# Performance work log

Hardware: AMD Instinct MI355X
Metric: run time of the kernel (lower is better)

Reference implementation:

```python
import jax, jax.numpy as jnp
import numpy as np

N_HEADS = 16
R = 64  # number of latents; note: scale = r**-0.5 per original code


def setup_inputs() -> dict:
    key = jax.random.key(0)
    ks = jax.random.split(key, 8)
    B, S, D = 32, 4096, 1024
    s = D ** -0.5
    return {
        "x": jax.random.normal(ks[0], (B, S, D), dtype=jnp.float32),
        "wq": jax.random.normal(ks[1], (D, D), dtype=jnp.float32) * s,
        "kv_latent": jax.random.normal(ks[2], (R, D), dtype=jnp.float32),
        "wo": jax.random.normal(ks[3], (D, D), dtype=jnp.float32) * s,
        "w1": jax.random.normal(ks[4], (D, D), dtype=jnp.float32) * s,
        "b1": jnp.zeros((D,), dtype=jnp.float32),
        "w2": jax.random.normal(ks[5], (D, D), dtype=jnp.float32) * s,
        "b2": jnp.zeros((D,), dtype=jnp.float32),
    }


def reference(x, wq, kv_latent, wo, w1, b1, w2, b2):
    B, S, D = x.shape
    hd = D // N_HEADS
    scale = R ** -0.5
    q = x.reshape(-1, D)                                   # [N, D], N = B*S
    xq = (q @ wq).reshape(-1, N_HEADS, hd) * scale         # [N, H, hd]
    kv = kv_latent.reshape(R, N_HEADS, hd)                 # [R, H, hd]
    attn = jax.nn.softmax(jnp.einsum('nhd,rhd->nhr', xq, kv), axis=-1)
    out = jnp.einsum('nhr,rhd->nhd', attn, kv).reshape(-1, D)
    out = out @ wo                                         # [N, D]
    # residual MLP block (exact GELU, matching torch nn.GELU default)
    h = jax.nn.gelu(out @ w1 + b1, approximate=False)
    out = h @ w2 + b2 + out
    # mean-pool per segment; equal segments of length S -> equivalent to
    # block_diag(ones(l)/l) @ out without materializing the [B, N] mask
    return out.reshape(B, S, D).mean(axis=1)               # [B, D]
```

## Files before the change

kernel.cpp:

```cpp
#include <hip/hip_runtime.h>

using bf16x8 = __attribute__((ext_vector_type(8))) __bf16;
using f32x4  = __attribute__((ext_vector_type(4))) float;

#define AS1(p) ((const __attribute__((address_space(1))) void*)(p))
#define AS3(p) ((__attribute__((address_space(3))) void*)(p))

__device__ __forceinline__ unsigned short f2bf(float f) {
  unsigned u = __float_as_uint(f);
  u += 0x7fffu + ((u >> 16) & 1u);
  return (unsigned short)(u >> 16);
}
__device__ __forceinline__ float bf2f(unsigned short h) {
  return __uint_as_float(((unsigned)h) << 16);
}

__global__ __launch_bounds__(256) void transpose_w(
    const float* __restrict__ wq, const float* __restrict__ wo,
    const float* __restrict__ w1, const float* __restrict__ w2,
    unsigned short* __restrict__ wqT, unsigned short* __restrict__ woT,
    unsigned short* __restrict__ w1T, unsigned short* __restrict__ w2T) {
  __shared__ float tile[64][65];
  const int z = blockIdx.z;
  const float* src = z == 0 ? wq : z == 1 ? wo : z == 2 ? w1 : w2;
  unsigned short* dst = z == 0 ? wqT : z == 1 ? woT : z == 2 ? w1T : w2T;
  const int tx = threadIdx.x & 63, ty = threadIdx.x >> 6;
  const int n0 = blockIdx.x * 64, k0 = blockIdx.y * 64;
#pragma unroll
  for (int i = 0; i < 16; i++) {
    int k = ty * 16 + i;
    tile[k][tx] = src[(size_t)(k0 + k) * 1024 + n0 + tx];
  }
  __syncthreads();
#pragma unroll
  for (int i = 0; i < 16; i++) {
    int n = ty * 16 + i;
    dst[(size_t)(n0 + n) * 1024 + k0 + tx] = f2bf(tile[tx][n]);
  }
}

__global__ __launch_bounds__(256) void convert_kv(
    const float* __restrict__ kv, unsigned short* __restrict__ kvb,
    unsigned short* __restrict__ kvT) {
  int idx = blockIdx.x * 256 + threadIdx.x;
  kvb[idx] = f2bf(kv[idx]);
  int h = idx >> 12, d = (idx >> 6) & 63, r = idx & 63;
  kvT[idx] = f2bf(kv[r * 1024 + h * 64 + d]);
}

template <int EPI, bool AF32>
__global__ __launch_bounds__(256) void gemm128(
    const void* __restrict__ Ap, const unsigned short* __restrict__ BT,
    unsigned short* __restrict__ C, const float* __restrict__ bias,
    const unsigned short* __restrict__ resid, float* __restrict__ pool,
    float scale) {
  __shared__ unsigned short As[128 * 32];
  __shared__ unsigned short Bs[128 * 32];
  const int tid = threadIdx.x;
  const int lane = tid & 63, wave = tid >> 6;
  const int wr = wave >> 1, wc = wave & 1;
  const int l15 = lane & 15, l4 = lane >> 4;
  const int bid = blockIdx.y * 8 + blockIdx.x;
  const int xcd = bid & 7, j = bid >> 3;
  const int row0 = ((xcd << 7) | (j >> 3)) * 128;
  const int col0 = (j & 7) * 128;
  const int swz = (l15 >> 1) & 3;

  f32x4 acc[4][4];
#pragma unroll
  for (int i = 0; i < 4; i++)
#pragma unroll
    for (int jj = 0; jj < 4; jj++) acc[i][jj] = f32x4{0.f, 0.f, 0.f, 0.f};

  for (int k0 = 0; k0 < 1024; k0 += 32) {
    if (AF32) {
      const float* A = (const float*)Ap;
#pragma unroll
      for (int s = 0; s < 4; s++) {
        int c = tid + 256 * s;
        int r = c >> 3, c4 = c & 7;
        const float4 v = *(const float4*)(A + (size_t)(row0 + r) * 1024 + k0 + c4 * 4);
        ushort4 b;
        b.x = f2bf(v.x); b.y = f2bf(v.y); b.z = f2bf(v.z); b.w = f2bf(v.w);
        int cc = (c4 >> 1) ^ ((r >> 1) & 3), h = c4 & 1;
        *(ushort4*)(As + r * 32 + cc * 8 + h * 4) = b;
      }
    } else {
      const unsigned short* A = (const unsigned short*)Ap;
#pragma unroll
      for (int t = 0; t < 2; t++) {
        int p = wave * 128 + t * 64 + lane;
        int r = p >> 2, c = (p & 3) ^ ((r >> 1) & 3);
        __builtin_amdgcn_global_load_lds(AS1(A + (size_t)(row0 + r) * 1024 + k0 + c * 8),
                                         AS3(As + p * 8), 16, 0, 0);
      }
    }
#pragma unroll
    for (int t = 0; t < 2; t++) {
      int p = wave * 128 + t * 64 + lane;
      int r = p >> 2, c = (p & 3) ^ ((r >> 1) & 3);
      __builtin_amdgcn_global_load_lds(AS1(BT + (size_t)(col0 + r) * 1024 + k0 + c * 8),
                                       AS3(Bs + p * 8), 16, 0, 0);
    }
    __syncthreads();

    bf16x8 af[4], bfr[4];
#pragma unroll
    for (int i = 0; i < 4; i++)
      af[i] = *(const bf16x8*)(As + (wr * 64 + i * 16 + l15) * 32 + (l4 ^ swz) * 8);
#pragma unroll
    for (int jj = 0; jj < 4; jj++)
      bfr[jj] = *(const bf16x8*)(Bs + (wc * 64 + jj * 16 + l15) * 32 + (l4 ^ swz) * 8);
#pragma unroll
    for (int i = 0; i < 4; i++)
#pragma unroll
      for (int jj = 0; jj < 4; jj++)
        acc[i][jj] = __builtin_amdgcn_mfma_f32_16x16x32_bf16(af[i], bfr[jj], acc[i][jj], 0, 0, 0);
    __syncthreads();
  }

  if (EPI == 0) {
#pragma unroll
    for (int i = 0; i < 4; i++)
#pragma unroll
      for (int jj = 0; jj < 4; jj++)
#pragma unroll
        for (int v = 0; v < 4; v++) {
          int row = row0 + wr * 64 + i * 16 + l4 * 4 + v;
          int col = col0 + wc * 64 + jj * 16 + l15;
          C[(size_t)row * 1024 + col] = f2bf(acc[i][jj][v] * scale);
        }
  } else if (EPI == 1) {
#pragma unroll
    for (int jj = 0; jj < 4; jj++) {
      int col = col0 + wc * 64 + jj * 16 + l15;
      float bj = bias[col];
#pragma unroll
      for (int i = 0; i < 4; i++)
#pragma unroll
        for (int v = 0; v < 4; v++) {
          int row = row0 + wr * 64 + i * 16 + l4 * 4 + v;
          float val = acc[i][jj][v] + bj;
          float g = 0.5f * val * (1.0f + erff(val * 0.70710678118654752f));
          C[(size_t)row * 1024 + col] = f2bf(g);
        }
    }
  } else {
    float cs[4] = {0.f, 0.f, 0.f, 0.f};
#pragma unroll
    for (int jj = 0; jj < 4; jj++) {
      int col = col0 + wc * 64 + jj * 16 + l15;
      float bj = bias[col];
#pragma unroll
      for (int i = 0; i < 4; i++)
#pragma unroll
        for (int v = 0; v < 4; v++) {
          int row = row0 + wr * 64 + i * 16 + l4 * 4 + v;
          float val = acc[i][jj][v] + bj + bf2f(resid[(size_t)row * 1024 + col]);
          cs[jj] += val;
        }
    }
#pragma unroll
    for (int jj = 0; jj < 4; jj++) {
      cs[jj] += __shfl_xor(cs[jj], 16);
      cs[jj] += __shfl_xor(cs[jj], 32);
    }
    if (l4 == 0) {
      int b = row0 >> 12;
#pragma unroll
      for (int jj = 0; jj < 4; jj++) {
        int col = col0 + wc * 64 + jj * 16 + l15;
        atomicAdd(pool + b * 1024 + col, cs[jj] * (1.0f / 4096.0f));
      }
    }
  }
}

__global__ __launch_bounds__(256) void attn_kernel(
    const unsigned short* __restrict__ q, const unsigned short* __restrict__ kvb,
    const unsigned short* __restrict__ kvT, unsigned short* __restrict__ outp) {
  __shared__ unsigned short smem[32768];
  unsigned short* qs   = smem;
  unsigned short* kvs  = smem + 16384;
  unsigned short* kvTs = smem + 24576;
  const int tid = threadIdx.x;
  const int lane = tid & 63, wave = tid >> 6;
  const int wr = wave >> 1, wc = wave & 1;
  const int l15 = lane & 15, l4 = lane >> 4;
  const int hp = blockIdx.x, row0 = blockIdx.y * 128;

#pragma unroll
  for (int t = 0; t < 8; t++) {
    int c = wave * 512 + t * 64 + lane;
    int r = c >> 4, c8 = c & 15;
    __builtin_amdgcn_global_load_lds(AS1(q + (size_t)(row0 + r) * 1024 + hp * 128 + c8 * 8),
                                     AS3(qs + (wave * 512 + t * 64) * 8), 16, 0, 0);
  }
#pragma unroll
  for (int t = 0; t < 4; t++) {
    int c = wave * 256 + t * 64 + lane;
    int h = c >> 9, r = (c >> 3) & 63, c8 = c & 7;
    __builtin_amdgcn_global_load_lds(AS1(kvb + r * 1024 + (hp * 2 + h) * 64 + c8 * 8),
                                     AS3(kvs + (wave * 256 + t * 64) * 8), 16, 0, 0);
    __builtin_amdgcn_global_load_lds(AS1(kvT + (hp * 2 + h) * 4096 + (c & 511) * 8),
                                     AS3(kvTs + (wave * 256 + t * 64) * 8), 16, 0, 0);
  }
  __syncthreads();

  f32x4 sc[4][4];
#pragma unroll
  for (int i = 0; i < 4; i++)
#pragma unroll
    for (int j = 0; j < 4; j++) sc[i][j] = f32x4{0.f, 0.f, 0.f, 0.f};
#pragma unroll
  for (int ks = 0; ks < 2; ks++) {
    bf16x8 af[4], bfr[4];
#pragma unroll
    for (int i = 0; i < 4; i++)
      af[i] = *(const bf16x8*)(qs + (wr * 64 + i * 16 + l15) * 128 + wc * 64 + ks * 32 + l4 * 8);
#pragma unroll
    for (int j = 0; j < 4; j++)
      bfr[j] = *(const bf16x8*)(kvs + wc * 4096 + (j * 16 + l15) * 64 + ks * 32 + l4 * 8);
#pragma unroll
    for (int i = 0; i < 4; i++)
#pragma unroll
      for (int j = 0; j < 4; j++)
        sc[i][j] = __builtin_amdgcn_mfma_f32_16x16x32_bf16(af[i], bfr[j], sc[i][j], 0, 0, 0);
  }
  __syncthreads();

  unsigned short* attn = qs;
#pragma unroll
  for (int i = 0; i < 4; i++)
#pragma unroll
    for (int v = 0; v < 4; v++) {
      float m = fmaxf(fmaxf(sc[i][0][v], sc[i][1][v]), fmaxf(sc[i][2][v], sc[i][3][v]));
#pragma unroll
      for (int msk = 1; msk <= 8; msk <<= 1) m = fmaxf(m, __shfl_xor(m, msk));
      float e0 = __expf(sc[i][0][v] - m), e1 = __expf(sc[i][1][v] - m);
      float e2 = __expf(sc[i][2][v] - m), e3 = __expf(sc[i][3][v] - m);
      float s = e0 + e1 + e2 + e3;
#pragma unroll
      for (int msk = 1; msk <= 8; msk <<= 1) s += __shfl_xor(s, msk);
      float inv = 1.0f / s;
      int row = wr * 64 + i * 16 + l4 * 4 + v;
      attn[wc * 8192 + row * 64 + 0 * 16 + l15] = f2bf(e0 * inv);
      attn[wc * 8192 + row * 64 + 1 * 16 + l15] = f2bf(e1 * inv);
      attn[wc * 8192 + row * 64 + 2 * 16 + l15] = f2bf(e2 * inv);
      attn[wc * 8192 + row * 64 + 3 * 16 + l15] = f2bf(e3 * inv);
    }

  f32x4 o[4][4];
#pragma unroll
  for (int i = 0; i < 4; i++)
#pragma unroll
    for (int j = 0; j < 4; j++) o[i][j] = f32x4{0.f, 0.f, 0.f, 0.f};
#pragma unroll
  for (int ks = 0; ks < 2; ks++) {
    bf16x8 af[4], bfr[4];
#pragma unroll
    for (int i = 0; i < 4; i++)
      af[i] = *(const bf16x8*)(attn + wc * 8192 + (wr * 64 + i * 16 + l15) * 64 + ks * 32 + l4 * 8);
#pragma unroll
    for (int j = 0; j < 4; j++)
      bfr[j] = *(const bf16x8*)(kvTs + wc * 4096 + (j * 16 + l15) * 64 + ks * 32 + l4 * 8);
#pragma unroll
    for (int i = 0; i < 4; i++)
#pragma unroll
      for (int j = 0; j < 4; j++)
        o[i][j] = __builtin_amdgcn_mfma_f32_16x16x32_bf16(af[i], bfr[j], o[i][j], 0, 0, 0);
  }
#pragma unroll
  for (int i = 0; i < 4; i++)
#pragma unroll
    for (int j = 0; j < 4; j++)
#pragma unroll
      for (int v = 0; v < 4; v++) {
        int row = row0 + wr * 64 + i * 16 + l4 * 4 + v;
        int col = (hp * 2 + wc) * 64 + j * 16 + l15;
        outp[(size_t)row * 1024 + col] = f2bf(o[i][j][v]);
      }
}

extern "C" void kernel_launch(void* const* d_in, const int* in_sizes, int n_in,
                              void* d_out, int out_size, void* d_ws, size_t ws_size,
                              hipStream_t stream) {
  const float* x  = (const float*)d_in[0];
  const float* wq = (const float*)d_in[1];
  const float* kv = (const float*)d_in[2];
  const float* wo = (const float*)d_in[3];
  const float* w1 = (const float*)d_in[4];
  const float* b1 = (const float*)d_in[5];
  const float* w2 = (const float*)d_in[6];
  const float* b2 = (const float*)d_in[7];
  char* ws = (char*)d_ws;
  const size_t MB = 1024 * 1024;
  unsigned short* wqT = (unsigned short*)(ws + 0 * MB);
  unsigned short* woT = (unsigned short*)(ws + 2 * MB);
  unsigned short* w1T = (unsigned short*)(ws + 4 * MB);
  unsigned short* w2T = (unsigned short*)(ws + 6 * MB);
  unsigned short* kvb = (unsigned short*)(ws + 8 * MB);
  unsigned short* kvT = (unsigned short*)(ws + 8 * MB + 256 * 1024);
  unsigned short* buf1 = (unsigned short*)(ws + 16 * MB);
  unsigned short* buf2 = (unsigned short*)(ws + 16 * MB + 256 * MB);
  float* out = (float*)d_out;

  hipMemsetAsync(d_out, 0, (size_t)out_size * sizeof(float), stream);
  transpose_w<<<dim3(16, 16, 4), 256, 0, stream>>>(wq, wo, w1, w2, wqT, woT, w1T, w2T);
  convert_kv<<<256, 256, 0, stream>>>(kv, kvb, kvT);

  dim3 g(8, 1024);
  gemm128<0, true ><<<g, 256, 0, stream>>>(x, wqT, buf1, nullptr, nullptr, nullptr, 0.125f);
  attn_kernel<<<g, 256, 0, stream>>>(buf1, kvb, kvT, buf2);
  gemm128<0, false><<<g, 256, 0, stream>>>(buf2, woT, buf1, nullptr, nullptr, nullptr, 1.0f);
  gemm128<1, false><<<g, 256, 0, stream>>>(buf1, w1T, buf2, b1, nullptr, nullptr, 1.0f);
  gemm128<2, false><<<g, 256, 0, stream>>>(buf2, w2T, nullptr, b2, buf1, out, 1.0f);
}
```

Measured before the change: 2.438 ms.

## Replace 128x128 GEMM with double-buffered 256x256 tile GEMM and pre-convert x

Replaces the 128x128, 256-thread GEMM with a 256x256-tile, 512-thread kernel that uses a 64-wide K step, an XOR-swizzled LDS layout and double-buffered global-to-LDS loads overlapped with MFMA compute. Wave priority is raised around the MFMA bursts. The fp32 input x is now converted to bf16 by a separate kernel so every GEMM uses the async LDS load path. This targets low arithmetic intensity and exposed load latency, at the cost of an extra pass over x, 128 KB of LDS per block and higher register pressure.

Measured after the change: 2.348 ms. 3.7% less time.

```diff
diff --git a/kernel.cpp b/kernel.cpp
--- a/kernel.cpp
+++ b/kernel.cpp
@@ -48,99 +48,142 @@
   kvT[idx] = f2bf(kv[r * 1024 + h * 64 + d]);
 }
 
-template <int EPI, bool AF32>
-__global__ __launch_bounds__(256) void gemm128(
-    const void* __restrict__ Ap, const unsigned short* __restrict__ BT,
+__global__ __launch_bounds__(256) void convert_x(
+    const float4* __restrict__ x, ushort4* __restrict__ xb) {
+  size_t i = (size_t)blockIdx.x * 256 + threadIdx.x;
+  float4 v = x[i];
+  ushort4 b;
+  b.x = f2bf(v.x); b.y = f2bf(v.y); b.z = f2bf(v.z); b.w = f2bf(v.w);
+  xb[i] = b;
+}
+
+template <int EPI>
+__global__ __launch_bounds__(512, 2) void gemm256(
+    const unsigned short* __restrict__ A, const unsigned short* __restrict__ BT,
     unsigned short* __restrict__ C, const float* __restrict__ bias,
     const unsigned short* __restrict__ resid, float* __restrict__ pool,
     float scale) {
-  __shared__ unsigned short As[128 * 32];
-  __shared__ unsigned short Bs[128 * 32];
+  __shared__ unsigned short Asm[2 * 16384];
+  __shared__ unsigned short Bsm[2 * 16384];
   const int tid = threadIdx.x;
   const int lane = tid & 63, wave = tid >> 6;
-  const int wr = wave >> 1, wc = wave & 1;
+  const int wr = wave >> 2, wc = wave & 3;
   const int l15 = lane & 15, l4 = lane >> 4;
-  const int bid = blockIdx.y * 8 + blockIdx.x;
-  const int xcd = bid & 7, j = bid >> 3;
-  const int row0 = ((xcd << 7) | (j >> 3)) * 128;
-  const int col0 = (j & 7) * 128;
-  const int swz = (l15 >> 1) & 3;
-
-  f32x4 acc[4][4];
-#pragma unroll
-  for (int i = 0; i < 4; i++)
-#pragma unroll
-    for (int jj = 0; jj < 4; jj++) acc[i][jj] = f32x4{0.f, 0.f, 0.f, 0.f};
-
-  for (int k0 = 0; k0 < 1024; k0 += 32) {
-    if (AF32) {
-      const float* A = (const float*)Ap;
-#pragma unroll
-      for (int s = 0; s < 4; s++) {
-        int c = tid + 256 * s;
-        int r = c >> 3, c4 = c & 7;
-        const float4 v = *(const float4*)(A + (size_t)(row0 + r) * 1024 + k0 + c4 * 4);
-        ushort4 b;
-        b.x = f2bf(v.x); b.y = f2bf(v.y); b.z = f2bf(v.z); b.w = f2bf(v.w);
-        int cc = (c4 >> 1) ^ ((r >> 1) & 3), h = c4 & 1;
-        *(ushort4*)(As + r * 32 + cc * 8 + h * 4) = b;
-      }
-    } else {
-      const unsigned short* A = (const unsigned short*)Ap;
-#pragma unroll
-      for (int t = 0; t < 2; t++) {
-        int p = wave * 128 + t * 64 + lane;
-        int r = p >> 2, c = (p & 3) ^ ((r >> 1) & 3);
-        __builtin_amdgcn_global_load_lds(AS1(A + (size_t)(row0 + r) * 1024 + k0 + c * 8),
-                                         AS3(As + p * 8), 16, 0, 0);
-      }
-    }
-#pragma unroll
-    for (int t = 0; t < 2; t++) {
-      int p = wave * 128 + t * 64 + lane;
-      int r = p >> 2, c = (p & 3) ^ ((r >> 1) & 3);
-      __builtin_amdgcn_global_load_lds(AS1(BT + (size_t)(col0 + r) * 1024 + k0 + c * 8),
-                                       AS3(Bs + p * 8), 16, 0, 0);
-    }
-    __syncthreads();
-
-    bf16x8 af[4], bfr[4];
-#pragma unroll
-    for (int i = 0; i < 4; i++)
-      af[i] = *(const bf16x8*)(As + (wr * 64 + i * 16 + l15) * 32 + (l4 ^ swz) * 8);
-#pragma unroll
-    for (int jj = 0; jj < 4; jj++)
-      bfr[jj] = *(const bf16x8*)(Bs + (wc * 64 + jj * 16 + l15) * 32 + (l4 ^ swz) * 8);
-#pragma unroll
-    for (int i = 0; i < 4; i++)
-#pragma unroll
-      for (int jj = 0; jj < 4; jj++)
-        acc[i][jj] = __builtin_amdgcn_mfma_f32_16x16x32_bf16(af[i], bfr[jj], acc[i][jj], 0, 0, 0);
-    __syncthreads();
-  }
+
+  const int bid = blockIdx.x;
+  const int idx = bid >> 3;
+  const int row0 = ((bid & 7) * 64 + (idx >> 2)) * 256;
+  const int col0 = (idx & 3) * 256;
+
+  const unsigned short* aSrc[4];
+  const unsigned short* bSrc[4];
+#pragma unroll
+  for (int s = 0; s < 4; s++) {
+    int p = tid + 512 * s;
+    int r = p >> 3, c = (p & 7) ^ (r & 7);
+    aSrc[s] = A  + (size_t)(row0 + r) * 1024 + c * 8;
+    bSrc[s] = BT + (size_t)(col0 + r) * 1024 + c * 8;
+  }
+
+  auto stage = [&](int t, int b) {
+#pragma unroll
+    for (int s = 0; s < 4; s++)
+      __builtin_amdgcn_global_load_lds(AS1(aSrc[s] + t * 64),
+                                       AS3(Asm + b * 16384 + (tid + 512 * s) * 8), 16, 0, 0);
+#pragma unroll
+    for (int s = 0; s < 4; s++)
+      __builtin_amdgcn_global_load_lds(AS1(bSrc[s] + t * 64),
+                                       AS3(Bsm + b * 16384 + (tid + 512 * s) * 8), 16, 0, 0);
+  };
+
+  f32x4 acc[8][4];
+#pragma unroll
+  for (int i = 0; i < 8; i++)
+#pragma unroll
+    for (int j = 0; j < 4; j++) acc[i][j] = f32x4{0.f, 0.f, 0.f, 0.f};
+
+  int aOff[8], bOff[4];
+#pragma unroll
+  for (int i = 0; i < 8; i++) {
+    int ra = wr * 128 + i * 16 + l15;
+    aOff[i] = ra * 64 + ((l4 ^ (ra & 7)) * 8);
+  }
+#pragma unroll
+  for (int j = 0; j < 4; j++) {
+    int rb = wc * 64 + j * 16 + l15;
+    bOff[j] = rb * 64 + ((l4 ^ (rb & 7)) * 8);
+  }
+
+  auto compute = [&](int b) {
+#pragma unroll
+    for (int ks = 0; ks < 2; ks++) {
+      bf16x8 af[8], bfr[4];
+#pragma unroll
+      for (int i = 0; i < 8; i++)
+        af[i] = *(const bf16x8*)(Asm + b * 16384 + (aOff[i] ^ (ks * 32)));
+#pragma unroll
+      for (int j = 0; j < 4; j++)
+        bfr[j] = *(const bf16x8*)(Bsm + b * 16384 + (bOff[j] ^ (ks * 32)));
+      __builtin_amdgcn_s_setprio(1);
+#pragma unroll
+      for (int i = 0; i < 8; i++)
+#pragma unroll
+        for (int j = 0; j < 4; j++)
+          acc[i][j] = __builtin_amdgcn_mfma_f32_16x16x32_bf16(af[i], bfr[j], acc[i][j], 0, 0, 0);
+      __builtin_amdgcn_s_setprio(0);
+    }
+  };
+
+  stage(0, 0);
+  stage(1, 1);
+  asm volatile("s_waitcnt vmcnt(8)" ::: "memory");
+  __builtin_amdgcn_sched_barrier(0);
+  __builtin_amdgcn_s_barrier();
+  __builtin_amdgcn_sched_barrier(0);
+
+  int cur = 0;
+#pragma unroll 2
+  for (int t = 0; t < 14; ++t) {
+    compute(cur);
+    __builtin_amdgcn_sched_barrier(0);
+    __builtin_amdgcn_s_barrier();
+    __builtin_amdgcn_sched_barrier(0);
+    stage(t + 2, cur);
+    asm volatile("s_waitcnt vmcnt(8)" ::: "memory");
+    __builtin_amdgcn_sched_barrier(0);
+    __builtin_amdgcn_s_barrier();
+    __builtin_amdgcn_sched_barrier(0);
+    cur ^= 1;
+  }
+  compute(cur);
+  asm volatile("s_waitcnt vmcnt(0)" ::: "memory");
+  __builtin_amdgcn_sched_barrier(0);
+  __builtin_amdgcn_s_barrier();
+  __builtin_amdgcn_sched_barrier(0);
+  compute(cur ^ 1);
 
   if (EPI == 0) {
 #pragma unroll
-    for (int i = 0; i < 4; i++)
-#pragma unroll
-      for (int jj = 0; jj < 4; jj++)
+    for (int i = 0; i < 8; i++)
+#pragma unroll
+      for (int j = 0; j < 4; j++)
 #pragma unroll
         for (int v = 0; v < 4; v++) {
-          int row = row0 + wr * 64 + i * 16 + l4 * 4 + v;
-          int col = col0 + wc * 64 + jj * 16 + l15;
-          C[(size_t)row * 1024 + col] = f2bf(acc[i][jj][v] * scale);
+          int row = row0 + wr * 128 + i * 16 + l4 * 4 + v;
+          int col = col0 + wc * 64 + j * 16 + l15;
+          C[(size_t)row * 1024 + col] = f2bf(acc[i][j][v] * scale);
         }
   } else if (EPI == 1) {
 #pragma unroll
-    for (int jj = 0; jj < 4; jj++) {
-      int col = col0 + wc * 64 + jj * 16 + l15;
+    for (int j = 0; j < 4; j++) {
+      int col = col0 + wc * 64 + j * 16 + l15;
       float bj = bias[col];
 #pragma unroll
-      for (int i = 0; i < 4; i++)
+      for (int i = 0; i < 8; i++)
 #pragma unroll
         for (int v = 0; v < 4; v++) {
-          int row = row0 + wr * 64 + i * 16 + l4 * 4 + v;
-          float val = acc[i][jj][v] + bj;
+          int row = row0 + wr * 128 + i * 16 + l4 * 4 + v;
+          float val = acc[i][j][v] + bj;
           float g = 0.5f * val * (1.0f + erff(val * 0.70710678118654752f));
           C[(size_t)row * 1024 + col] = f2bf(g);
         }
@@ -148,29 +191,29 @@
   } else {
     float cs[4] = {0.f, 0.f, 0.f, 0.f};
 #pragma unroll
-    for (int jj = 0; jj < 4; jj++) {
-      int col = col0 + wc * 64 + jj * 16 + l15;
+    for (int j = 0; j < 4; j++) {
+      int col = col0 + wc * 64 + j * 16 + l15;
       float bj = bias[col];
 #pragma unroll
-      for (int i = 0; i < 4; i++)
+      for (int i = 0; i < 8; i++)
 #pragma unroll
         for (int v = 0; v < 4; v++) {
-          int row = row0 + wr * 64 + i * 16 + l4 * 4 + v;
-          float val = acc[i][jj][v] + bj + bf2f(resid[(size_t)row * 1024 + col]);
-          cs[jj] += val;
+          int row = row0 + wr * 128 + i * 16 + l4 * 4 + v;
+          float val = acc[i][j][v] + bj + bf2f(resid[(size_t)row * 1024 + col]);
+          cs[j] += val;
         }
     }
 #pragma unroll
-    for (int jj = 0; jj < 4; jj++) {
-      cs[jj] += __shfl_xor(cs[jj], 16);
-      cs[jj] += __shfl_xor(cs[jj], 32);
+    for (int j = 0; j < 4; j++) {
+      cs[j] += __shfl_xor(cs[j], 16);
+      cs[j] += __shfl_xor(cs[j], 32);
     }
     if (l4 == 0) {
       int b = row0 >> 12;
 #pragma unroll
-      for (int jj = 0; jj < 4; jj++) {
-        int col = col0 + wc * 64 + jj * 16 + l15;
-        atomicAdd(pool + b * 1024 + col, cs[jj] * (1.0f / 4096.0f));
+      for (int j = 0; j < 4; j++) {
+        int col = col0 + wc * 64 + j * 16 + l15;
+        atomicAdd(pool + b * 1024 + col, cs[j] * (1.0f / 4096.0f));
       }
     }
   }
@@ -308,11 +351,11 @@
   hipMemsetAsync(d_out, 0, (size_t)out_size * sizeof(float), stream);
   transpose_w<<<dim3(16, 16, 4), 256, 0, stream>>>(wq, wo, w1, w2, wqT, woT, w1T, w2T);
   convert_kv<<<256, 256, 0, stream>>>(kv, kvb, kvT);
-
-  dim3 g(8, 1024);
-  gemm128<0, true ><<<g, 256, 0, stream>>>(x, wqT, buf1, nullptr, nullptr, nullptr, 0.125f);
-  attn_kernel<<<g, 256, 0, stream>>>(buf1, kvb, kvT, buf2);
-  gemm128<0, false><<<g, 256, 0, stream>>>(buf2, woT, buf1, nullptr, nullptr, nullptr, 1.0f);
-  gemm128<1, false><<<g, 256, 0, stream>>>(buf1, w1T, buf2, b1, nullptr, nullptr, 1.0f);
-  gemm128<2, false><<<g, 256, 0, stream>>>(buf2, w2T, nullptr, b2, buf1, out, 1.0f);
-}
+  convert_x<<<131072, 256, 0, stream>>>((const float4*)x, (ushort4*)buf2);
+
+  gemm256<0><<<2048, 512, 0, stream>>>(buf2, wqT, buf1, nullptr, nullptr, nullptr, 0.125f);
+  attn_kernel<<<dim3(8, 1024), 256, 0, stream>>>(buf1, kvb, kvT, buf2);
+  gemm256<0><<<2048, 512, 0, stream>>>(buf2, woT, buf1, nullptr, nullptr, nullptr, 1.0f);
+  gemm256<1><<<2048, 512, 0, stream>>>(buf1, w1T, buf2, b1, nullptr, nullptr, 1.0f);
+  gemm256<2><<<2048, 512, 0, stream>>>(buf2, w2T, nullptr, b2, buf1, out, 1.0f);
+}
```
